# Optimization experiments

Measured on AMD Instinct MI355X. Metric: run time of the kernel, lower is better.

Reference implementation:

```python
import jax, jax.numpy as jnp
from jax import lax
import numpy as np

N_LAYERS = 8
N_NODES = 200000
N_CHILD = 32


def setup_inputs() -> dict:
    key = jax.random.key(0)
    k1, k2, k3 = jax.random.split(key, 3)
    X = jax.random.normal(k1, (N_NODES,), dtype=jnp.float32)
    w = jnp.ones((1,), dtype=jnp.float32)
    child_idx = jax.random.randint(k2, (N_LAYERS, N_NODES, N_CHILD), 0, N_NODES, dtype=jnp.int32)
    fun_ids = jax.random.randint(k3, (N_LAYERS, N_NODES), 0, 4, dtype=jnp.int32)
    return {"X": X, "w": w, "child_idx": child_idx, "fun_ids": fun_ids}


def _apply_act(fid, x):
    # per-node activation dispatch: 0=tanh, 1=sigmoid, 2=relu, 3=identity
    return jnp.select(
        [fid == 0, fid == 1, fid == 2],
        [jnp.tanh(x), jax.nn.sigmoid(x), jax.nn.relu(x)],
        x,
    )


def reference(X, w, child_idx, fun_ids):
    # Layer 0 values are the raw inputs X; each subsequent layer computes
    # fun(best_w * sum(child values))  (params = w * ones(K), so dot == w * sum)
    def step(vals, layer):
        ci, fi = layer  # ci: [N, K] indices into previous layer's vals; fi: [N]
        inp = w[0] * jnp.sum(vals[ci], axis=-1)  # gather children + weighted sum
        return _apply_act(fi, inp), None

    out, _ = lax.scan(step, X, (child_idx, fun_ids))
    return out  # values of the final (output) layer, shape [N_NODES]
```

## Files before the change

kernel.cpp:

```cpp
#include <hip/hip_runtime.h>

#define N_NODES  200000
#define N_CHILD  32
#define N_LAYERS 8
#define CHUNK    40000
#define NCHUNK   5
#define NB       256
#define NPB      782
#define BT       832
#define NWAVE    (BT / 64)
#define W16      (CHUNK / 8)
#define NSEG     ((W16 + 63) / 64)

#define AS1 __attribute__((address_space(1)))
#define AS3 __attribute__((address_space(3)))

__device__ __forceinline__ void stage_window_async(const ushort* __restrict__ src,
                                                   ushort* dst, int wave, int lane)
{
    #pragma unroll
    for (int sg = 0; sg < (NSEG + NWAVE - 1) / NWAVE; ++sg) {
        const int seg = wave + sg * NWAVE;
        const int e   = (seg << 6) + lane;
        if (seg < NSEG && e < W16) {
            __builtin_amdgcn_global_load_lds(
                (const AS1 void*)(const void*)(src + (size_t)e * 8),
                (AS3 void*)(void*)(dst + (size_t)e * 8),
                16, 0, 0);
        }
    }
}

__device__ __forceinline__ ushort f32_to_bf16_rne(float x) {
    unsigned u = __builtin_bit_cast(unsigned, x);
    u += 0x7FFFu + ((u >> 16) & 1u);
    return (ushort)(u >> 16);
}

__global__ __launch_bounds__(1024) void cvt_kernel(const float4* __restrict__ x4,
                                                   ushort4* __restrict__ o4) {
    const int i = blockIdx.x * 1024 + threadIdx.x;
    if (i < N_NODES / 4) {
        float4 v = x4[i];
        ushort4 r;
        r.x = f32_to_bf16_rne(v.x); r.y = f32_to_bf16_rne(v.y);
        r.z = f32_to_bf16_rne(v.z); r.w = f32_to_bf16_rne(v.w);
        o4[i] = r;
    }
}

template<bool LAST>
__global__ __launch_bounds__(BT) void layer_kernel(
    const ushort* __restrict__ vals_in,
    void*         __restrict__ vals_out,
    const int*    __restrict__ child_idx,
    const int*    __restrict__ fun_ids,
    const float*  __restrict__ wptr)
{
    __shared__ __align__(16) ushort lds[2][CHUNK];
    const int tid    = threadIdx.x;
    const int wave   = tid >> 6;
    const int lane   = tid & 63;
    const int node   = blockIdx.x * NPB + tid;
    const bool active = (tid < NPB) && (node < N_NODES);

    stage_window_async(vals_in, lds[0], wave, lane);

    int idx[N_CHILD];
    int fid = 3;
    if (active) {
        const int4* ci = (const int4*)(child_idx + (size_t)node * N_CHILD);
        #pragma unroll
        for (int j = 0; j < N_CHILD / 4; ++j) {
            int4 c = ci[j];
            idx[4*j+0] = c.x; idx[4*j+1] = c.y;
            idx[4*j+2] = c.z; idx[4*j+3] = c.w;
        }
        fid = fun_ids[node];
    } else {
        #pragma unroll
        for (int j = 0; j < N_CHILD; ++j) idx[j] = 0;
    }

    __syncthreads();

    float s = 0.0f;
    #pragma unroll 1
    for (int c = 0; c < NCHUNK; ++c) {
        if (c + 1 < NCHUNK)
            stage_window_async(vals_in + (size_t)(c + 1) * CHUNK,
                               lds[(c + 1) & 1], wave, lane);

        const ushort* __restrict__ buf = lds[c & 1];
        const unsigned cbase = (unsigned)(c * CHUNK);
        #pragma unroll
        for (int j = 0; j < N_CHILD; ++j) {
            unsigned off = (unsigned)idx[j] - cbase;
            bool in   = off < (unsigned)CHUNK;
            ushort rw = buf[in ? off : 0u];
            float v   = __builtin_bit_cast(float, (unsigned)rw << 16);
            s += in ? v : 0.0f;
        }
        __syncthreads();
    }

    if (active) {
        float x = wptr[0] * s;
        float y;
        if (fid == 0)      y = tanhf(x);
        else if (fid == 1) y = 1.0f / (1.0f + __expf(-x));
        else if (fid == 2) y = fmaxf(x, 0.0f);
        else               y = x;
        if (LAST) ((float*)vals_out)[node]  = y;
        else      ((ushort*)vals_out)[node] = f32_to_bf16_rne(y);
    }
}

extern "C" void kernel_launch(void* const* d_in, const int* in_sizes, int n_in,
                              void* d_out, int out_size, void* d_ws, size_t ws_size,
                              hipStream_t stream) {
    const float* X         = (const float*)d_in[0];
    const float* w         = (const float*)d_in[1];
    const int*   child_idx = (const int*)d_in[2];
    const int*   fun_ids   = (const int*)d_in[3];
    float*       out       = (float*)d_out;
    ushort*      bufA      = (ushort*)d_ws;
    ushort*      bufB      = (ushort*)((char*)d_ws + 512000);

    cvt_kernel<<<(N_NODES / 4 + 1023) / 1024, 1024, 0, stream>>>(
        (const float4*)X, (ushort4*)bufA);

    const ushort* cur = bufA;
    for (int l = 0; l < N_LAYERS; ++l) {
        const int*   ci = child_idx + (size_t)l * N_NODES * N_CHILD;
        const int*   fi = fun_ids   + (size_t)l * N_NODES;
        if (l == N_LAYERS - 1) {
            layer_kernel<true><<<NB, BT, 0, stream>>>(cur, (void*)out, ci, fi, w);
        } else {
            ushort* nxt = (l & 1) ? bufA : bufB;
            layer_kernel<false><<<NB, BT, 0, stream>>>(cur, (void*)nxt, ci, fi, w);
            cur = nxt;
        }
    }
}
```

Before: 388.8 us.

## Fuse all layers into one cooperative kernel and prefetch next-layer indices

Replaces the conversion kernel and the eight per-layer launches with a single cooperative kernel that uses grid-wide syncs between layers. While each layer's chunk loop runs, the child indices and function ids for the next layer are loaded in the background so their latency overlaps the LDS gather. This removes per-launch overhead and the index-load stall at the start of each layer. In exchange it needs a second 32-entry index register array, which raises register pressure, and it depends on all 256 blocks of 832 threads being co-resident.

```diff
diff --git a/kernel.cpp b/kernel.cpp
--- a/kernel.cpp
+++ b/kernel.cpp
@@ -1,4 +1,7 @@
 #include <hip/hip_runtime.h>
+#include <hip/hip_cooperative_groups.h>
+
+namespace cg = cooperative_groups;
 
 #define N_NODES  200000
 #define N_CHILD  32
@@ -37,82 +40,115 @@
     return (ushort)(u >> 16);
 }
 
-__global__ __launch_bounds__(1024) void cvt_kernel(const float4* __restrict__ x4,
-                                                   ushort4* __restrict__ o4) {
-    const int i = blockIdx.x * 1024 + threadIdx.x;
-    if (i < N_NODES / 4) {
-        float4 v = x4[i];
-        ushort4 r;
-        r.x = f32_to_bf16_rne(v.x); r.y = f32_to_bf16_rne(v.y);
-        r.z = f32_to_bf16_rne(v.z); r.w = f32_to_bf16_rne(v.w);
-        o4[i] = r;
-    }
-}
-
-template<bool LAST>
-__global__ __launch_bounds__(BT) void layer_kernel(
-    const ushort* __restrict__ vals_in,
-    void*         __restrict__ vals_out,
-    const int*    __restrict__ child_idx,
-    const int*    __restrict__ fun_ids,
-    const float*  __restrict__ wptr)
+__global__ __launch_bounds__(BT) void fused_kernel(
+    const float* __restrict__ X,
+    float*       __restrict__ out_f32,
+    ushort*      __restrict__ bufA,
+    ushort*      __restrict__ bufB,
+    const int*   __restrict__ child_idx,
+    const int*   __restrict__ fun_ids,
+    const float* __restrict__ wptr)
 {
+    cg::grid_group grid = cg::this_grid();
     __shared__ __align__(16) ushort lds[2][CHUNK];
     const int tid    = threadIdx.x;
     const int wave   = tid >> 6;
     const int lane   = tid & 63;
     const int node   = blockIdx.x * NPB + tid;
     const bool active = (tid < NPB) && (node < N_NODES);
+    const float w0   = wptr[0];
 
-    stage_window_async(vals_in, lds[0], wave, lane);
+    const int gtid = blockIdx.x * BT + tid;
+    if (gtid < N_NODES / 4) {
+        float4 v = ((const float4*)X)[gtid];
+        ushort4 r;
+        r.x = f32_to_bf16_rne(v.x); r.y = f32_to_bf16_rne(v.y);
+        r.z = f32_to_bf16_rne(v.z); r.w = f32_to_bf16_rne(v.w);
+        ((ushort4*)bufA)[gtid] = r;
+    }
 
-    int idx[N_CHILD];
-    int fid = 3;
+    int idxA[N_CHILD], idxB[N_CHILD];
+    int fidA = 3, fidB = 3;
     if (active) {
         const int4* ci = (const int4*)(child_idx + (size_t)node * N_CHILD);
         #pragma unroll
         for (int j = 0; j < N_CHILD / 4; ++j) {
             int4 c = ci[j];
-            idx[4*j+0] = c.x; idx[4*j+1] = c.y;
-            idx[4*j+2] = c.z; idx[4*j+3] = c.w;
+            idxA[4*j+0] = c.x; idxA[4*j+1] = c.y;
+            idxA[4*j+2] = c.z; idxA[4*j+3] = c.w;
         }
-        fid = fun_ids[node];
+        fidA = fun_ids[node];
     } else {
         #pragma unroll
-        for (int j = 0; j < N_CHILD; ++j) idx[j] = 0;
+        for (int j = 0; j < N_CHILD; ++j) idxA[j] = 0;
     }
+    #pragma unroll
+    for (int j = 0; j < N_CHILD; ++j) idxB[j] = 0;
 
-    __syncthreads();
+    grid.sync();
 
-    float s = 0.0f;
+    auto layer_body = [&](int l, int (&idxC)[N_CHILD], int fidC,
+                          int (&idxN)[N_CHILD], int& fidN) {
+        const ushort* __restrict__ cur = (l & 1) ? bufB : bufA;
+        stage_window_async(cur, lds[0], wave, lane);
+        __syncthreads();
+
+        const size_t nlbase = (size_t)((l + 1 < N_LAYERS) ? l + 1 : l) * N_NODES;
+        const int4* cin = (const int4*)(child_idx + nlbase * N_CHILD + (size_t)node * N_CHILD);
+
+        float s = 0.0f;
+        #pragma unroll 1
+        for (int c = 0; c < NCHUNK; ++c) {
+            if (c + 1 < NCHUNK)
+                stage_window_async(cur + (size_t)(c + 1) * CHUNK,
+                                   lds[(c + 1) & 1], wave, lane);
+
+            int4 pa, pb;
+            const bool pf = (l + 1 < N_LAYERS) && (c < 4) && active;
+            if (pf) {
+                pa = cin[2 * c];
+                pb = cin[2 * c + 1];
+                if (c == 0) fidN = fun_ids[nlbase + node];
+            }
+
+            const ushort* __restrict__ buf = lds[c & 1];
+            const unsigned cbase = (unsigned)(c * CHUNK);
+            #pragma unroll
+            for (int j = 0; j < N_CHILD; ++j) {
+                unsigned off = (unsigned)idxC[j] - cbase;
+                bool in   = off < (unsigned)CHUNK;
+                ushort rw = buf[in ? off : 0u];
+                float v   = __builtin_bit_cast(float, (unsigned)rw << 16);
+                s += in ? v : 0.0f;
+            }
+
+            if (pf) {
+                idxN[8*c+0] = pa.x; idxN[8*c+1] = pa.y; idxN[8*c+2] = pa.z; idxN[8*c+3] = pa.w;
+                idxN[8*c+4] = pb.x; idxN[8*c+5] = pb.y; idxN[8*c+6] = pb.z; idxN[8*c+7] = pb.w;
+            }
+            __syncthreads();
+        }
+
+        if (active) {
+            float x = w0 * s;
+            float y;
+            if (fidC == 0)      y = tanhf(x);
+            else if (fidC == 1) y = 1.0f / (1.0f + __expf(-x));
+            else if (fidC == 2) y = fmaxf(x, 0.0f);
+            else                y = x;
+            if (l == N_LAYERS - 1) out_f32[node] = y;
+            else {
+                ushort* nxt = (l & 1) ? bufA : bufB;
+                nxt[node] = f32_to_bf16_rne(y);
+            }
+        }
+        if (l + 1 < N_LAYERS) grid.sync();
+    };
+
     #pragma unroll 1
-    for (int c = 0; c < NCHUNK; ++c) {
-        if (c + 1 < NCHUNK)
-            stage_window_async(vals_in + (size_t)(c + 1) * CHUNK,
-                               lds[(c + 1) & 1], wave, lane);
-
-        const ushort* __restrict__ buf = lds[c & 1];
-        const unsigned cbase = (unsigned)(c * CHUNK);
-        #pragma unroll
-        for (int j = 0; j < N_CHILD; ++j) {
-            unsigned off = (unsigned)idx[j] - cbase;
-            bool in   = off < (unsigned)CHUNK;
-            ushort rw = buf[in ? off : 0u];
-            float v   = __builtin_bit_cast(float, (unsigned)rw << 16);
-            s += in ? v : 0.0f;
-        }
-        __syncthreads();
-    }
-
-    if (active) {
-        float x = wptr[0] * s;
-        float y;
-        if (fid == 0)      y = tanhf(x);
-        else if (fid == 1) y = 1.0f / (1.0f + __expf(-x));
-        else if (fid == 2) y = fmaxf(x, 0.0f);
-        else               y = x;
-        if (LAST) ((float*)vals_out)[node]  = y;
-        else      ((ushort*)vals_out)[node] = f32_to_bf16_rne(y);
+    for (int lp = 0; lp < N_LAYERS / 2; ++lp) {
+        layer_body(2 * lp,     idxA, fidA, idxB, fidB);
+        layer_body(2 * lp + 1, idxB, fidB, idxA, fidA);
     }
 }
 
@@ -127,19 +163,8 @@
     ushort*      bufA      = (ushort*)d_ws;
     ushort*      bufB      = (ushort*)((char*)d_ws + 512000);
 
-    cvt_kernel<<<(N_NODES / 4 + 1023) / 1024, 1024, 0, stream>>>(
-        (const float4*)X, (ushort4*)bufA);
-
-    const ushort* cur = bufA;
-    for (int l = 0; l < N_LAYERS; ++l) {
-        const int*   ci = child_idx + (size_t)l * N_NODES * N_CHILD;
-        const int*   fi = fun_ids   + (size_t)l * N_NODES;
-        if (l == N_LAYERS - 1) {
-            layer_kernel<true><<<NB, BT, 0, stream>>>(cur, (void*)out, ci, fi, w);
-        } else {
-            ushort* nxt = (l & 1) ? bufA : bufB;
-            layer_kernel<false><<<NB, BT, 0, stream>>>(cur, (void*)nxt, ci, fi, w);
-            cur = nxt;
-        }
-    }
+    void* args[] = { (void*)&X, (void*)&out, (void*)&bufA, (void*)&bufB,
+                     (void*)&child_idx, (void*)&fun_ids, (void*)&w };
+    hipLaunchCooperativeKernel((void*)fused_kernel, dim3(NB), dim3(BT),
+                               args, 0, stream);
 }
```

Measured after the change: 718.1 us. 1.85x slower.
